# Optimization experiments

Measured on AMD Instinct MI355X. Metric: run time of the kernel, lower is better.

## Reference

```python
import jax, jax.numpy as jnp
import numpy as np

N_NODES = 50000


def gcn_conv(x, W, b, src, dst, n):
    """PyG GCNConv: add self-loops, sym-normalize, linear, scatter-add."""
    loop = jnp.arange(n, dtype=src.dtype)
    s = jnp.concatenate([src, loop])  # [E+N]
    d = jnp.concatenate([dst, loop])
    deg = jax.ops.segment_sum(jnp.ones_like(s, dtype=x.dtype), d, num_segments=n)
    dinv = jnp.where(deg > 0, jax.lax.rsqrt(deg), 0.0)  # deg^-1/2
    norm = dinv[s] * dinv[d]  # [E+N]
    h = x @ W  # [N, out] dense GEMM first (in >= out)
    msg = h[s] * norm[:, None]  # gather + scale
    out = jax.ops.segment_sum(msg, d, num_segments=n)  # scatter-add
    return out + b


def setup_inputs() -> dict:
    key = jax.random.key(0)
    k1, k2, k3, k4, k5, k6, k7, k8 = jax.random.split(key, 8)
    in_c, hid_c, out_c = 512, 128, 64
    n, e, l = N_NODES, 800000, 100000
    x = jax.random.normal(k1, (n, in_c), dtype=jnp.float32)
    edge_index = jax.random.randint(k2, (2, e), 0, n, dtype=jnp.int64)
    edge_label_index = jax.random.randint(k3, (2, l), 0, n, dtype=jnp.int64)
    # Glorot-ish init for weights, zeros for biases (PyG default bias=zeros)
    W1 = jax.random.normal(k4, (in_c, hid_c), dtype=jnp.float32) / np.sqrt(in_c)
    b1 = jnp.zeros((hid_c,), dtype=jnp.float32)
    W2 = jax.random.normal(k5, (hid_c, out_c), dtype=jnp.float32) / np.sqrt(hid_c)
    b2 = jnp.zeros((out_c,), dtype=jnp.float32)
    return {"x": x, "edge_index": edge_index, "edge_label_index": edge_label_index,
            "W1": W1, "b1": b1, "W2": W2, "b2": b2}


def reference(x, edge_index, edge_label_index, W1, b1, W2, b2):
    n = x.shape[0]
    src, dst = edge_index[0], edge_index[1]
    z = jax.nn.relu(gcn_conv(x, W1, b1, src, dst, n))
    z = gcn_conv(z, W2, b2, src, dst, n)
    es, ed = edge_label_index[0], edge_label_index[1]
    return jnp.sum(z[es] * z[ed], axis=-1).reshape(-1)
```

## Files before the change

### kernel.cpp

```cpp
#include <hip/hip_runtime.h>

#define IN_C  512
#define HID_C 128
#define OUT_C 64

using short8 = __attribute__((ext_vector_type(8))) short;
using floatx4 = __attribute__((ext_vector_type(4))) float;

__device__ inline unsigned short f2bf(float f) {
    unsigned u = __builtin_bit_cast(unsigned, f);
    u += 0x7FFFu + ((u >> 16) & 1u);
    return (unsigned short)(u >> 16);
}
__device__ inline float bf2f(unsigned short h) {
    unsigned u = ((unsigned)h) << 16;
    return __builtin_bit_cast(float, u);
}

__global__ void k_zero_int(int* __restrict__ p, int n) {
    int i = blockIdx.x * blockDim.x + threadIdx.x;
    if (i < n) p[i] = 0;
}

__global__ void k_count(const int* __restrict__ dst, int* __restrict__ cnt, int e) {
    int i = blockIdx.x * blockDim.x + threadIdx.x;
    if (i < e) atomicAdd(&cnt[dst[i]], 1);
}

__global__ void k_dinv(const int* __restrict__ cnt, float* __restrict__ dinv, int n) {
    int i = blockIdx.x * blockDim.x + threadIdx.x;
    if (i < n) dinv[i] = rsqrtf(1.0f + (float)cnt[i]);
}

__global__ void k_blocksum(const int* __restrict__ cnt, int* __restrict__ bsum, int n) {
    __shared__ int sdata[256];
    int t = threadIdx.x;
    int i = blockIdx.x * 256 + t;
    sdata[t] = (i < n) ? cnt[i] : 0;
    __syncthreads();
    for (int s = 128; s > 0; s >>= 1) {
        if (t < s) sdata[t] += sdata[t + s];
        __syncthreads();
    }
    if (t == 0) bsum[blockIdx.x] = sdata[0];
}

__global__ void k_scanpartials(int* __restrict__ bsum, int nb) {
    __shared__ int sdata[256];
    int t = threadIdx.x;
    int orig = (t < nb) ? bsum[t] : 0;
    sdata[t] = orig;
    __syncthreads();
    for (int off = 1; off < 256; off <<= 1) {
        int v = (t >= off) ? sdata[t - off] : 0;
        __syncthreads();
        sdata[t] += v;
        __syncthreads();
    }
    if (t < nb) bsum[t] = sdata[t] - orig;
}

__global__ void k_scanfinal(const int* __restrict__ cnt, const int* __restrict__ bsum_ex,
                            int* __restrict__ row_ptr, int n, int e_total) {
    __shared__ int sdata[256];
    int t = threadIdx.x;
    int i = blockIdx.x * 256 + t;
    int orig = (i < n) ? cnt[i] : 0;
    sdata[t] = orig;
    __syncthreads();
    for (int off = 1; off < 256; off <<= 1) {
        int v = (t >= off) ? sdata[t - off] : 0;
        __syncthreads();
        sdata[t] += v;
        __syncthreads();
    }
    if (i < n) row_ptr[i] = sdata[t] - orig + bsum_ex[blockIdx.x];
    if (i == 0) row_ptr[n] = e_total;
}

__global__ void k_fill(const int* __restrict__ src, const int* __restrict__ dst,
                       const int* __restrict__ row_ptr, int* __restrict__ cur,
                       int* __restrict__ col, int e) {
    int i = blockIdx.x * blockDim.x + threadIdx.x;
    if (i < e) {
        int d = dst[i];
        int pos = atomicAdd(&cur[d], 1);
        col[row_ptr[d] + pos] = src[i];
    }
}

__global__ void k_prep_w(const float* __restrict__ W, unsigned short* __restrict__ hi,
                         unsigned short* __restrict__ lo, int K, int N) {
    int i = blockIdx.x * blockDim.x + threadIdx.x;
    if (i >= K * N) return;
    int k = i / N, n = i % N;
    float v = W[i];
    unsigned short h = f2bf(v);
    float r = v - bf2f(h);
    hi[(long)n * K + k] = h;
    lo[(long)n * K + k] = f2bf(r);
}

template <int K, int NPW>
__global__ __launch_bounds__(256) void k_gemm_mfma(
    const float* __restrict__ A, const unsigned short* __restrict__ Bt_hi,
    const unsigned short* __restrict__ Bt_lo, const float* __restrict__ dinv,
    float* __restrict__ Hs, int M) {
    constexpr int N = 64 * NPW;
    constexpr int LDA = 72;
    constexpr int NT = K / 64;
    __shared__ __align__(16) unsigned short As_hi[2][64 * LDA];
    __shared__ __align__(16) unsigned short As_lo[2][64 * LDA];

    const int tid = threadIdx.x;
    const int w = tid >> 6;
    const int lane = tid & 63;
    const int m = lane & 15;
    const int quad = lane >> 4;
    const int m0 = blockIdx.x * 64;

    const int srow = tid >> 4;
    const int skk = (tid & 15) << 2;

    floatx4 acc[4][NPW];
#pragma unroll
    for (int mi = 0; mi < 4; ++mi)
#pragma unroll
        for (int ni = 0; ni < NPW; ++ni) acc[mi][ni] = (floatx4){0.f, 0.f, 0.f, 0.f};

    float4 pf[4];
#pragma unroll
    for (int i = 0; i < 4; ++i) {
        int gm = m0 + srow + 16 * i;
        pf[i] = make_float4(0.f, 0.f, 0.f, 0.f);
        if (gm < M) pf[i] = *(const float4*)&A[(long)gm * K + skk];
    }
#pragma unroll
    for (int i = 0; i < 4; ++i) {
        ushort4 h, l;
        h.x = f2bf(pf[i].x); l.x = f2bf(pf[i].x - bf2f(h.x));
        h.y = f2bf(pf[i].y); l.y = f2bf(pf[i].y - bf2f(h.y));
        h.z = f2bf(pf[i].z); l.z = f2bf(pf[i].z - bf2f(h.z));
        h.w = f2bf(pf[i].w); l.w = f2bf(pf[i].w - bf2f(h.w));
        int off = (srow + 16 * i) * LDA + skk;
        *(ushort4*)&As_hi[0][off] = h;
        *(ushort4*)&As_lo[0][off] = l;
    }

    for (int t = 0; t < NT; ++t) {
        __syncthreads();
        const int buf = t & 1;
        if (t + 1 < NT) {
#pragma unroll
            for (int i = 0; i < 4; ++i) {
                int gm = m0 + srow + 16 * i;
                pf[i] = make_float4(0.f, 0.f, 0.f, 0.f);
                if (gm < M) pf[i] = *(const float4*)&A[(long)gm * K + (t + 1) * 64 + skk];
            }
        }
#pragma unroll
        for (int s = 0; s < 2; ++s) {
            short8 ah[4], al[4];
#pragma unroll
            for (int mi = 0; mi < 4; ++mi) {
                int off = (mi * 16 + m) * LDA + s * 32 + quad * 8;
                ah[mi] = *(const short8*)&As_hi[buf][off];
                al[mi] = *(const short8*)&As_lo[buf][off];
            }
#pragma unroll
            for (int ni = 0; ni < NPW; ++ni) {
                int n = (w * NPW + ni) * 16 + m;
                long boff = (long)n * K + t * 64 + s * 32 + quad * 8;
                short8 bh = *(const short8*)&Bt_hi[boff];
                short8 bl = *(const short8*)&Bt_lo[boff];
#pragma unroll
                for (int mi = 0; mi < 4; ++mi) {
                    acc[mi][ni] = __builtin_amdgcn_mfma_f32_16x16x32_bf16(ah[mi], bh, acc[mi][ni], 0, 0, 0);
                    acc[mi][ni] = __builtin_amdgcn_mfma_f32_16x16x32_bf16(ah[mi], bl, acc[mi][ni], 0, 0, 0);
                    acc[mi][ni] = __builtin_amdgcn_mfma_f32_16x16x32_bf16(al[mi], bh, acc[mi][ni], 0, 0, 0);
                }
            }
        }
        if (t + 1 < NT) {
#pragma unroll
            for (int i = 0; i < 4; ++i) {
                ushort4 h, l;
                h.x = f2bf(pf[i].x); l.x = f2bf(pf[i].x - bf2f(h.x));
                h.y = f2bf(pf[i].y); l.y = f2bf(pf[i].y - bf2f(h.y));
                h.z = f2bf(pf[i].z); l.z = f2bf(pf[i].z - bf2f(h.z));
                h.w = f2bf(pf[i].w); l.w = f2bf(pf[i].w - bf2f(h.w));
                int off = (srow + 16 * i) * LDA + skk;
                *(ushort4*)&As_hi[buf ^ 1][off] = h;
                *(ushort4*)&As_lo[buf ^ 1][off] = l;
            }
        }
    }

#pragma unroll
    for (int mi = 0; mi < 4; ++mi) {
#pragma unroll
        for (int r = 0; r < 4; ++r) {
            int row = m0 + mi * 16 + quad * 4 + r;
            if (row < M) {
                float dv = dinv[row];
#pragma unroll
                for (int ni = 0; ni < NPW; ++ni) {
                    int n = (w * NPW + ni) * 16 + m;
                    Hs[(long)row * N + n] = acc[mi][ni][r] * dv;
                }
            }
        }
    }
}

__global__ __launch_bounds__(256) void k_agg1(
    const float* __restrict__ h, const int* __restrict__ row_ptr,
    const int* __restrict__ col, const float* __restrict__ dinv,
    const float* __restrict__ bias, float* __restrict__ z, int n) {
    int node = blockIdx.x * 4 + (threadIdx.x >> 6);
    node = __builtin_amdgcn_readfirstlane(node);
    if (node >= n) return;
    int lane = threadIdx.x & 63;
    const float2* hp = (const float2*)h;
    float2 acc = hp[(long)node * 64 + lane];
    int rs = row_ptr[node], re = row_ptr[node + 1];
    int j = rs;
    for (; j + 4 <= re; j += 4) {
        int s0 = col[j], s1 = col[j + 1], s2 = col[j + 2], s3 = col[j + 3];
        float2 v0 = hp[(long)s0 * 64 + lane];
        float2 v1 = hp[(long)s1 * 64 + lane];
        float2 v2 = hp[(long)s2 * 64 + lane];
        float2 v3 = hp[(long)s3 * 64 + lane];
        acc.x += v0.x + v1.x + v2.x + v3.x;
        acc.y += v0.y + v1.y + v2.y + v3.y;
    }
    for (; j < re; ++j) {
        int s = col[j];
        float2 v = hp[(long)s * 64 + lane];
        acc.x += v.x;
        acc.y += v.y;
    }
    float dv = dinv[node];
    float2 b = ((const float2*)bias)[lane];
    acc.x = fmaxf(fmaf(acc.x, dv, b.x), 0.f);
    acc.y = fmaxf(fmaf(acc.y, dv, b.y), 0.f);
    ((float2*)z)[(long)node * 64 + lane] = acc;
}

__global__ __launch_bounds__(256) void k_agg2(
    const float* __restrict__ h, const int* __restrict__ row_ptr,
    const int* __restrict__ col, const float* __restrict__ dinv,
    const float* __restrict__ bias, float* __restrict__ z, int n) {
    int node = blockIdx.x * 4 + (threadIdx.x >> 6);
    node = __builtin_amdgcn_readfirstlane(node);
    if (node >= n) return;
    int lane = threadIdx.x & 63;
    float acc = h[(long)node * 64 + lane];
    int rs = row_ptr[node], re = row_ptr[node + 1];
    int j = rs;
    for (; j + 4 <= re; j += 4) {
        int s0 = col[j], s1 = col[j + 1], s2 = col[j + 2], s3 = col[j + 3];
        acc += h[(long)s0 * 64 + lane] + h[(long)s1 * 64 + lane] +
               h[(long)s2 * 64 + lane] + h[(long)s3 * 64 + lane];
    }
    for (; j < re; ++j) acc += h[(long)col[j] * 64 + lane];
    z[(long)node * 64 + lane] = fmaf(acc, dinv[node], bias[lane]);
}

__global__ void k_dot(const float* __restrict__ z2, const int* __restrict__ es,
                      const int* __restrict__ ed, float* __restrict__ out, int L) {
    int gid = blockIdx.x * blockDim.x + threadIdx.x;
    int wid = gid >> 6;
    int lane = threadIdx.x & 63;
    if (wid >= L) return;
    int a = es[wid], b = ed[wid];
    float v = z2[(long)a * OUT_C + lane] * z2[(long)b * OUT_C + lane];
#pragma unroll
    for (int off = 32; off > 0; off >>= 1) v += __shfl_down(v, off);
    if (lane == 0) out[wid] = v;
}

extern "C" void kernel_launch(void* const* d_in, const int* in_sizes, int n_in,
                              void* d_out, int out_size, void* d_ws, size_t ws_size,
                              hipStream_t stream) {
    const float* x = (const float*)d_in[0];
    const int* ei = (const int*)d_in[1];
    const int* eli = (const int*)d_in[2];
    const float* W1 = (const float*)d_in[3];
    const float* b1 = (const float*)d_in[4];
    const float* W2 = (const float*)d_in[5];
    const float* b2 = (const float*)d_in[6];
    float* out = (float*)d_out;

    const int N = in_sizes[0] / IN_C;
    const int E = in_sizes[1] / 2;
    const int L = in_sizes[2] / 2;
    const int* src = ei;
    const int* dst = ei + E;
    const int* es = eli;
    const int* ed = eli + L;

    const int Npad = (N + 63) & ~63;
    const int Epad = (E + 3) & ~3;

    int* cnt = (int*)d_ws;
    int* cur = cnt + Npad;
    int* row_ptr = cur + Npad;
    int* bsum = row_ptr + Npad + 64;
    int* col = bsum + 256;
    float* dinv = (float*)(col + Epad);
    float* h1s = dinv + Npad;
    float* z1 = h1s + (long)N * HID_C;
    float* h2s = h1s;
    float* z2 = h1s + (long)N * OUT_C;
    unsigned short* wt1_hi = (unsigned short*)(z1 + (long)N * HID_C);
    unsigned short* wt1_lo = wt1_hi + IN_C * HID_C;
    unsigned short* wt2_hi = wt1_lo + IN_C * HID_C;
    unsigned short* wt2_lo = wt2_hi + HID_C * OUT_C;

    const int TPB = 256;
    const int nb = (N + 255) / 256;

    k_prep_w<<<(IN_C * HID_C + TPB - 1) / TPB, TPB, 0, stream>>>(W1, wt1_hi, wt1_lo, IN_C, HID_C);
    k_prep_w<<<(HID_C * OUT_C + TPB - 1) / TPB, TPB, 0, stream>>>(W2, wt2_hi, wt2_lo, HID_C, OUT_C);

    k_zero_int<<<(2 * Npad + TPB - 1) / TPB, TPB, 0, stream>>>(cnt, 2 * Npad);
    k_count<<<(E + TPB - 1) / TPB, TPB, 0, stream>>>(dst, cnt, E);
    k_dinv<<<(N + TPB - 1) / TPB, TPB, 0, stream>>>(cnt, dinv, N);
    k_blocksum<<<nb, 256, 0, stream>>>(cnt, bsum, N);
    k_scanpartials<<<1, 256, 0, stream>>>(bsum, nb);
    k_scanfinal<<<nb, 256, 0, stream>>>(cnt, bsum, row_ptr, N, E);
    k_fill<<<(E + TPB - 1) / TPB, TPB, 0, stream>>>(src, dst, row_ptr, cur, col, E);

    k_gemm_mfma<IN_C, 2><<<(N + 63) / 64, 256, 0, stream>>>(x, wt1_hi, wt1_lo, dinv, h1s, N);
    k_agg1<<<(N + 3) / 4, 256, 0, stream>>>(h1s, row_ptr, col, dinv, b1, z1, N);

    k_gemm_mfma<HID_C, 1><<<(N + 63) / 64, 256, 0, stream>>>(z1, wt2_hi, wt2_lo, dinv, h2s, N);
    k_agg2<<<(N + 3) / 4, 256, 0, stream>>>(h2s, row_ptr, col, dinv, b2, z2, N);

    k_dot<<<((long)L * 64 + TPB - 1) / TPB, TPB, 0, stream>>>(z2, es, ed, out, L);
}
```

Measured before the change: 405.0 us.

## Prefetch A tiles two steps ahead and use lighter LDS-only barriers in MFMA GEMM

Restructures the GEMM main loop so two register prefetch sets are in flight, issuing global loads for tile t+2 while tile t is computed. The loop is fully unrolled in pairs. The __syncthreads is replaced by a barrier that waits only on LDS counters, so outstanding global loads are not drained at each barrier. This is meant to hide global memory latency better, at the cost of more registers and possible lower occupancy.

After: 413.1 us. Within noise of the previous version (+2.0%).

```diff
diff --git a/kernel.cpp b/kernel.cpp
--- a/kernel.cpp
+++ b/kernel.cpp
@@ -109,6 +109,7 @@
     constexpr int N = 64 * NPW;
     constexpr int LDA = 72;
     constexpr int NT = K / 64;
+    static_assert((NT & 1) == 0, "NT must be even");
     __shared__ __align__(16) unsigned short As_hi[2][64 * LDA];
     __shared__ __align__(16) unsigned short As_lo[2][64 * LDA];
 
@@ -128,49 +129,43 @@
 #pragma unroll
         for (int ni = 0; ni < NPW; ++ni) acc[mi][ni] = (floatx4){0.f, 0.f, 0.f, 0.f};
 
-    float4 pf[4];
-#pragma unroll
-    for (int i = 0; i < 4; ++i) {
-        int gm = m0 + srow + 16 * i;
-        pf[i] = make_float4(0.f, 0.f, 0.f, 0.f);
-        if (gm < M) pf[i] = *(const float4*)&A[(long)gm * K + skk];
-    }
-#pragma unroll
-    for (int i = 0; i < 4; ++i) {
-        ushort4 h, l;
-        h.x = f2bf(pf[i].x); l.x = f2bf(pf[i].x - bf2f(h.x));
-        h.y = f2bf(pf[i].y); l.y = f2bf(pf[i].y - bf2f(h.y));
-        h.z = f2bf(pf[i].z); l.z = f2bf(pf[i].z - bf2f(h.z));
-        h.w = f2bf(pf[i].w); l.w = f2bf(pf[i].w - bf2f(h.w));
-        int off = (srow + 16 * i) * LDA + skk;
-        *(ushort4*)&As_hi[0][off] = h;
-        *(ushort4*)&As_lo[0][off] = l;
-    }
-
-    for (int t = 0; t < NT; ++t) {
-        __syncthreads();
-        const int buf = t & 1;
-        if (t + 1 < NT) {
-#pragma unroll
-            for (int i = 0; i < 4; ++i) {
-                int gm = m0 + srow + 16 * i;
-                pf[i] = make_float4(0.f, 0.f, 0.f, 0.f);
-                if (gm < M) pf[i] = *(const float4*)&A[(long)gm * K + (t + 1) * 64 + skk];
-            }
+    float4 pfA[4], pfB[4];
+
+    auto issue = [&](float4* pf, int t0) {
+#pragma unroll
+        for (int i = 0; i < 4; ++i) {
+            int gm = m0 + srow + 16 * i;
+            pf[i] = make_float4(0.f, 0.f, 0.f, 0.f);
+            if (t0 < NT && gm < M) pf[i] = *(const float4*)&A[(long)gm * K + t0 * 64 + skk];
         }
+    };
+    auto conv = [&](const float4* pf, int b) {
+#pragma unroll
+        for (int i = 0; i < 4; ++i) {
+            ushort4 h, l;
+            h.x = f2bf(pf[i].x); l.x = f2bf(pf[i].x - bf2f(h.x));
+            h.y = f2bf(pf[i].y); l.y = f2bf(pf[i].y - bf2f(h.y));
+            h.z = f2bf(pf[i].z); l.z = f2bf(pf[i].z - bf2f(h.z));
+            h.w = f2bf(pf[i].w); l.w = f2bf(pf[i].w - bf2f(h.w));
+            int off = (srow + 16 * i) * LDA + skk;
+            *(ushort4*)&As_hi[b][off] = h;
+            *(ushort4*)&As_lo[b][off] = l;
+        }
+    };
+    auto compute = [&](int b, int t0) {
 #pragma unroll
         for (int s = 0; s < 2; ++s) {
             short8 ah[4], al[4];
 #pragma unroll
             for (int mi = 0; mi < 4; ++mi) {
                 int off = (mi * 16 + m) * LDA + s * 32 + quad * 8;
-                ah[mi] = *(const short8*)&As_hi[buf][off];
-                al[mi] = *(const short8*)&As_lo[buf][off];
+                ah[mi] = *(const short8*)&As_hi[b][off];
+                al[mi] = *(const short8*)&As_lo[b][off];
             }
 #pragma unroll
             for (int ni = 0; ni < NPW; ++ni) {
                 int n = (w * NPW + ni) * 16 + m;
-                long boff = (long)n * K + t * 64 + s * 32 + quad * 8;
+                long boff = (long)n * K + t0 * 64 + s * 32 + quad * 8;
                 short8 bh = *(const short8*)&Bt_hi[boff];
                 short8 bl = *(const short8*)&Bt_lo[boff];
 #pragma unroll
@@ -181,19 +176,29 @@
                 }
             }
         }
-        if (t + 1 < NT) {
-#pragma unroll
-            for (int i = 0; i < 4; ++i) {
-                ushort4 h, l;
-                h.x = f2bf(pf[i].x); l.x = f2bf(pf[i].x - bf2f(h.x));
-                h.y = f2bf(pf[i].y); l.y = f2bf(pf[i].y - bf2f(h.y));
-                h.z = f2bf(pf[i].z); l.z = f2bf(pf[i].z - bf2f(h.z));
-                h.w = f2bf(pf[i].w); l.w = f2bf(pf[i].w - bf2f(h.w));
-                int off = (srow + 16 * i) * LDA + skk;
-                *(ushort4*)&As_hi[buf ^ 1][off] = h;
-                *(ushort4*)&As_lo[buf ^ 1][off] = l;
-            }
-        }
+    };
+    auto bar = [&]() {
+        asm volatile("" ::: "memory");
+        asm volatile("s_waitcnt lgkmcnt(0)" ::: "memory");
+        __builtin_amdgcn_s_barrier();
+        asm volatile("" ::: "memory");
+    };
+
+    issue(pfA, 0);
+    issue(pfB, 1);
+    conv(pfA, 0);
+    bar();
+
+#pragma unroll
+    for (int t = 0; t < NT; t += 2) {
+        issue(pfA, t + 2);
+        compute(0, t);
+        conv(pfB, 1);
+        bar();
+        issue(pfB, t + 3);
+        compute(1, t + 1);
+        if (t + 2 < NT) conv(pfA, 0);
+        bar();
     }
 
 #pragma unroll
```

## Store pre-aggregation features in fp16 and split neighbors across half-waves

Applied to the files above, without the earlier changes.

The GEMM epilogue now writes the dinv-scaled hidden features as fp16 instead of fp32, halving the bytes gathered per edge in both aggregation kernels. The aggregation kernels are reorganized so each half-wave processes alternate neighbors with wider per-lane loads, and the halves are combined with a shuffle before the bias/ReLU epilogue. The workspace layout is adjusted for the smaller buffers. This trades some precision (fp16 rounding of intermediate features) for lower gather bandwidth in the memory-bound sparse aggregation.

After: 380.1 us. -6.1%, faster.

```diff
diff --git a/kernel.cpp b/kernel.cpp
--- a/kernel.cpp
+++ b/kernel.cpp
@@ -15,6 +15,13 @@
 __device__ inline float bf2f(unsigned short h) {
     unsigned u = ((unsigned)h) << 16;
     return __builtin_bit_cast(float, u);
+}
+__device__ inline unsigned short f2h(float f) {
+    _Float16 h = (_Float16)f;
+    return __builtin_bit_cast(unsigned short, h);
+}
+__device__ inline float h2f(unsigned v) {
+    return (float)__builtin_bit_cast(_Float16, (unsigned short)v);
 }
 
 __global__ void k_zero_int(int* __restrict__ p, int n) {
@@ -105,7 +112,7 @@
 __global__ __launch_bounds__(256) void k_gemm_mfma(
     const float* __restrict__ A, const unsigned short* __restrict__ Bt_hi,
     const unsigned short* __restrict__ Bt_lo, const float* __restrict__ dinv,
-    float* __restrict__ Hs, int M) {
+    unsigned short* __restrict__ Hs, int M) {
     constexpr int N = 64 * NPW;
     constexpr int LDA = 72;
     constexpr int NT = K / 64;
@@ -206,7 +213,7 @@
 #pragma unroll
                 for (int ni = 0; ni < NPW; ++ni) {
                     int n = (w * NPW + ni) * 16 + m;
-                    Hs[(long)row * N + n] = acc[mi][ni][r] * dv;
+                    Hs[(long)row * N + n] = f2h(acc[mi][ni][r] * dv);
                 }
             }
         }
@@ -214,57 +221,112 @@
 }
 
 __global__ __launch_bounds__(256) void k_agg1(
-    const float* __restrict__ h, const int* __restrict__ row_ptr,
+    const unsigned short* __restrict__ h, const int* __restrict__ row_ptr,
     const int* __restrict__ col, const float* __restrict__ dinv,
     const float* __restrict__ bias, float* __restrict__ z, int n) {
     int node = blockIdx.x * 4 + (threadIdx.x >> 6);
     node = __builtin_amdgcn_readfirstlane(node);
     if (node >= n) return;
     int lane = threadIdx.x & 63;
-    const float2* hp = (const float2*)h;
-    float2 acc = hp[(long)node * 64 + lane];
+    int half = lane >> 5, li = lane & 31;
+    const uint2* hp = (const uint2*)h;
+    float4 acc = make_float4(0.f, 0.f, 0.f, 0.f);
+    if (half == 0) {
+        uint2 v = hp[(long)node * 32 + li];
+        acc.x = h2f(v.x); acc.y = h2f(v.x >> 16);
+        acc.z = h2f(v.y); acc.w = h2f(v.y >> 16);
+    }
     int rs = row_ptr[node], re = row_ptr[node + 1];
-    int j = rs;
-    for (; j + 4 <= re; j += 4) {
-        int s0 = col[j], s1 = col[j + 1], s2 = col[j + 2], s3 = col[j + 3];
-        float2 v0 = hp[(long)s0 * 64 + lane];
-        float2 v1 = hp[(long)s1 * 64 + lane];
-        float2 v2 = hp[(long)s2 * 64 + lane];
-        float2 v3 = hp[(long)s3 * 64 + lane];
-        acc.x += v0.x + v1.x + v2.x + v3.x;
-        acc.y += v0.y + v1.y + v2.y + v3.y;
-    }
-    for (; j < re; ++j) {
+    int cnt = re - rs, pairs = cnt >> 1;
+    int j = rs + half;
+    int p = 0;
+    for (; p + 4 <= pairs; p += 4, j += 8) {
+        int s0 = col[j], s1 = col[j + 2], s2 = col[j + 4], s3 = col[j + 6];
+        uint2 v0 = hp[(long)s0 * 32 + li];
+        uint2 v1 = hp[(long)s1 * 32 + li];
+        uint2 v2 = hp[(long)s2 * 32 + li];
+        uint2 v3 = hp[(long)s3 * 32 + li];
+        acc.x += h2f(v0.x) + h2f(v1.x) + h2f(v2.x) + h2f(v3.x);
+        acc.y += h2f(v0.x >> 16) + h2f(v1.x >> 16) + h2f(v2.x >> 16) + h2f(v3.x >> 16);
+        acc.z += h2f(v0.y) + h2f(v1.y) + h2f(v2.y) + h2f(v3.y);
+        acc.w += h2f(v0.y >> 16) + h2f(v1.y >> 16) + h2f(v2.y >> 16) + h2f(v3.y >> 16);
+    }
+    for (; p < pairs; ++p, j += 2) {
         int s = col[j];
-        float2 v = hp[(long)s * 64 + lane];
-        acc.x += v.x;
-        acc.y += v.y;
-    }
-    float dv = dinv[node];
-    float2 b = ((const float2*)bias)[lane];
-    acc.x = fmaxf(fmaf(acc.x, dv, b.x), 0.f);
-    acc.y = fmaxf(fmaf(acc.y, dv, b.y), 0.f);
-    ((float2*)z)[(long)node * 64 + lane] = acc;
+        uint2 v = hp[(long)s * 32 + li];
+        acc.x += h2f(v.x); acc.y += h2f(v.x >> 16);
+        acc.z += h2f(v.y); acc.w += h2f(v.y >> 16);
+    }
+    if ((cnt & 1) && half == 0) {
+        int s = col[re - 1];
+        uint2 v = hp[(long)s * 32 + li];
+        acc.x += h2f(v.x); acc.y += h2f(v.x >> 16);
+        acc.z += h2f(v.y); acc.w += h2f(v.y >> 16);
+    }
+    float ox = __shfl(acc.x, li + 32);
+    float oy = __shfl(acc.y, li + 32);
+    float oz = __shfl(acc.z, li + 32);
+    float ow = __shfl(acc.w, li + 32);
+    if (half == 0) {
+        acc.x += ox; acc.y += oy; acc.z += oz; acc.w += ow;
+        float dv = dinv[node];
+        float4 b = ((const float4*)bias)[li];
+        float4 o;
+        o.x = fmaxf(fmaf(acc.x, dv, b.x), 0.f);
+        o.y = fmaxf(fmaf(acc.y, dv, b.y), 0.f);
+        o.z = fmaxf(fmaf(acc.z, dv, b.z), 0.f);
+        o.w = fmaxf(fmaf(acc.w, dv, b.w), 0.f);
+        ((float4*)z)[(long)node * 32 + li] = o;
+    }
 }
 
 __global__ __launch_bounds__(256) void k_agg2(
-    const float* __restrict__ h, const int* __restrict__ row_ptr,
+    const unsigned short* __restrict__ h, const int* __restrict__ row_ptr,
     const int* __restrict__ col, const float* __restrict__ dinv,
     const float* __restrict__ bias, float* __restrict__ z, int n) {
     int node = blockIdx.x * 4 + (threadIdx.x >> 6);
     node = __builtin_amdgcn_readfirstlane(node);
     if (node >= n) return;
     int lane = threadIdx.x & 63;
-    float acc = h[(long)node * 64 + lane];
+    int half = lane >> 5, li = lane & 31;
+    const unsigned* hp = (const unsigned*)h;
+    float2 acc = make_float2(0.f, 0.f);
+    if (half == 0) {
+        unsigned v = hp[(long)node * 32 + li];
+        acc.x = h2f(v); acc.y = h2f(v >> 16);
+    }
     int rs = row_ptr[node], re = row_ptr[node + 1];
-    int j = rs;
-    for (; j + 4 <= re; j += 4) {
-        int s0 = col[j], s1 = col[j + 1], s2 = col[j + 2], s3 = col[j + 3];
-        acc += h[(long)s0 * 64 + lane] + h[(long)s1 * 64 + lane] +
-               h[(long)s2 * 64 + lane] + h[(long)s3 * 64 + lane];
-    }
-    for (; j < re; ++j) acc += h[(long)col[j] * 64 + lane];
-    z[(long)node * 64 + lane] = fmaf(acc, dinv[node], bias[lane]);
+    int cnt = re - rs, pairs = cnt >> 1;
+    int j = rs + half;
+    int p = 0;
+    for (; p + 4 <= pairs; p += 4, j += 8) {
+        int s0 = col[j], s1 = col[j + 2], s2 = col[j + 4], s3 = col[j + 6];
+        unsigned v0 = hp[(long)s0 * 32 + li];
+        unsigned v1 = hp[(long)s1 * 32 + li];
+        unsigned v2 = hp[(long)s2 * 32 + li];
+        unsigned v3 = hp[(long)s3 * 32 + li];
+        acc.x += h2f(v0) + h2f(v1) + h2f(v2) + h2f(v3);
+        acc.y += h2f(v0 >> 16) + h2f(v1 >> 16) + h2f(v2 >> 16) + h2f(v3 >> 16);
+    }
+    for (; p < pairs; ++p, j += 2) {
+        unsigned v = hp[(long)col[j] * 32 + li];
+        acc.x += h2f(v); acc.y += h2f(v >> 16);
+    }
+    if ((cnt & 1) && half == 0) {
+        unsigned v = hp[(long)col[re - 1] * 32 + li];
+        acc.x += h2f(v); acc.y += h2f(v >> 16);
+    }
+    float ox = __shfl(acc.x, li + 32);
+    float oy = __shfl(acc.y, li + 32);
+    if (half == 0) {
+        acc.x += ox; acc.y += oy;
+        float dv = dinv[node];
+        float2 b = ((const float2*)bias)[li];
+        float2 o;
+        o.x = fmaf(acc.x, dv, b.x);
+        o.y = fmaf(acc.y, dv, b.y);
+        ((float2*)z)[(long)node * 32 + li] = o;
+    }
 }
 
 __global__ void k_dot(const float* __restrict__ z2, const int* __restrict__ es,
@@ -309,11 +371,11 @@
     int* bsum = row_ptr + Npad + 64;
     int* col = bsum + 256;
     float* dinv = (float*)(col + Epad);
-    float* h1s = dinv + Npad;
-    float* z1 = h1s + (long)N * HID_C;
-    float* h2s = h1s;
-    float* z2 = h1s + (long)N * OUT_C;
-    unsigned short* wt1_hi = (unsigned short*)(z1 + (long)N * HID_C);
+    unsigned short* h1s = (unsigned short*)(dinv + Npad);
+    float* z1 = (float*)(h1s + (long)N * HID_C);
+    unsigned short* h2s = h1s;
+    float* z2 = z1 + (long)N * HID_C;
+    unsigned short* wt1_hi = (unsigned short*)(z2 + (long)N * OUT_C);
     unsigned short* wt1_lo = wt1_hi + IN_C * HID_C;
     unsigned short* wt2_hi = wt1_lo + IN_C * HID_C;
     unsigned short* wt2_lo = wt2_hi + HID_C * OUT_C;
```
